# Kernel tuning notes

Hardware: AMD Instinct MI355X
Metric: run time of the kernel (lower is better)

## Reference

```python
import jax, jax.numpy as jnp
import numpy as np

B, S, D_MODEL, H = 2, 2048, 1024, 16
HD = D_MODEL // H  # 64
THETA = 10000.0


def setup_inputs() -> dict:
    key = jax.random.key(0)
    ks = jax.random.split(key, 5)
    std = (2.0 / (D_MODEL + D_MODEL)) ** 0.5
    x = jax.random.normal(ks[0], (B, S, D_MODEL), dtype=jnp.float32)
    Wq = jax.random.normal(ks[1], (D_MODEL, D_MODEL), dtype=jnp.float32) * std
    Wk = jax.random.normal(ks[2], (D_MODEL, D_MODEL), dtype=jnp.float32) * std
    Wv = jax.random.normal(ks[3], (D_MODEL, D_MODEL), dtype=jnp.float32) * std
    Wo = jax.random.normal(ks[4], (D_MODEL, D_MODEL), dtype=jnp.float32) * std
    # RoPE tables (buffers)
    pos = jnp.arange(S, dtype=jnp.float32)
    freq = THETA ** (-jnp.arange(0, HD, 2, dtype=jnp.float32) / HD)  # [HD/2]
    ang = jnp.outer(pos, freq)  # [S, HD/2]
    token_positions = jnp.arange(S, dtype=jnp.int32)
    return {
        "x": x,
        "token_positions": token_positions,
        "use_rope": 1,
        "Wq": Wq, "Wk": Wk, "Wv": Wv, "Wo": Wo,
        "cos": jnp.cos(ang), "sin": jnp.sin(ang),
    }


def _apply_rope(t, c, sn):
    # t: [b,h,s,d]; c,sn: [s,d/2] (broadcast over b,h)
    e = t[..., 0::2]
    o = t[..., 1::2]
    return jnp.stack([e * c - o * sn, o * c + e * sn], axis=-1).reshape(t.shape)


def reference(x, token_positions, use_rope, Wq, Wk, Wv, Wo, cos, sin):
    b, s, _ = x.shape

    def split_heads(t):  # [b,s,D] -> [b,h,s,hd]
        return t.reshape(b, s, H, HD).transpose(0, 2, 1, 3)

    q = split_heads(x @ Wq.T)
    k = split_heads(x @ Wk.T)
    v = split_heads(x @ Wv.T)

    if use_rope:
        c = cos[token_positions]   # [s, hd/2]
        sn = sin[token_positions]  # [s, hd/2]
        q = _apply_rope(q, c, sn)
        k = _apply_rope(k, c, sn)

    scale = 1.0 / jnp.sqrt(jnp.float32(HD))
    scores = jnp.einsum('bhqd,bhkd->bhqk', q, k) * scale  # [b,h,s,s]
    causal = jnp.tril(jnp.ones((s, s), dtype=bool))
    scores = jnp.where(causal, scores, -jnp.inf)
    attn = jax.nn.softmax(scores, axis=-1)
    y = jnp.einsum('bhqk,bhkd->bhqd', attn, v)
    y = y.transpose(0, 2, 1, 3).reshape(b, s, D_MODEL)
    return y @ Wo.T
```

## Files before the change

### kernel.cpp

```cpp
#include <hip/hip_runtime.h>
#include <math.h>

#define BB 2
#define SS 2048
#define DM 1024
#define NH 16
#define HD 64

typedef __attribute__((ext_vector_type(8))) __bf16 bf16x8;
typedef __attribute__((ext_vector_type(4))) __bf16 bf16x4;
typedef __attribute__((ext_vector_type(8))) unsigned short u16x8;
typedef __attribute__((ext_vector_type(4))) float f32x4;
typedef unsigned short u16;
typedef unsigned int u32;
typedef __attribute__((address_space(1))) unsigned int u32g;
typedef __attribute__((address_space(3))) unsigned int u32l;

#define CEXP 0.18033688011112042f

static __device__ __forceinline__ u16 f2bf(float f) {
    __bf16 h = (__bf16)f;
    return __builtin_bit_cast(unsigned short, h);
}

static __device__ __forceinline__ void gld16(const u16* g, u16* l) {
    __builtin_amdgcn_global_load_lds((const u32g*)g, (u32l*)l, 16, 0, 0);
}

__global__ __launch_bounds__(256)
void cast_all(const float* __restrict__ x,
              const float* __restrict__ wq, const float* __restrict__ wk,
              const float* __restrict__ wv, const float* __restrict__ wo,
              u16* __restrict__ xb, u16* __restrict__ wqb, u16* __restrict__ wkb,
              u16* __restrict__ wvb, u16* __restrict__ wob)
{
    const int N4X = (BB * SS * DM) / 4;
    const int N4W = (DM * DM) / 4;
    int i = blockIdx.x * 256 + threadIdx.x;
    const float* src; u16* dst; int off;
    if (i < N4X) { src = x; dst = xb; off = i; }
    else {
        int i2 = i - N4X;
        int w = i2 >> 18;
        off = i2 & (N4W - 1);
        switch (w) {
            case 0:  src = wq; dst = wqb; break;
            case 1:  src = wk; dst = wkb; break;
            case 2:  src = wv; dst = wvb; break;
            default: src = wo; dst = wob; break;
        }
    }
    float4 v = ((const float4*)src)[off];
    ushort4 o;
    o.x = f2bf(v.x); o.y = f2bf(v.y); o.z = f2bf(v.z); o.w = f2bf(v.w);
    ((ushort4*)dst)[off] = o;
}

__global__ __launch_bounds__(256)
void qkv_gemm(const u16* __restrict__ X,
              const u16* __restrict__ Wq, const u16* __restrict__ Wk,
              const u16* __restrict__ Wv,
              u16* __restrict__ Q, u16* __restrict__ K, u16* __restrict__ V)
{
    const u16* W; u16* dst;
    if (blockIdx.z == 0)      { W = Wq; dst = Q; }
    else if (blockIdx.z == 1) { W = Wk; dst = K; }
    else                      { W = Wv; dst = V; }

    __shared__ u16 As[128 * 32];
    __shared__ u16 Bs[128 * 32];
    const int t  = threadIdx.x;
    const int wv = t >> 6, L = t & 63, ln = L & 15, qd = L >> 4;
    const int i0 = blockIdx.y * 128, j0 = blockIdx.x * 128;
    const int wm = (wv >> 1) * 64, wn = (wv & 1) * 64;
    const int srow = L >> 2, scol = (L & 3) * 8;

    f32x4 acc[4][4];
    #pragma unroll
    for (int a = 0; a < 4; ++a)
        #pragma unroll
        for (int b = 0; b < 4; ++b)
            #pragma unroll
            for (int e = 0; e < 4; ++e) acc[a][b][e] = 0.f;

    for (int k0 = 0; k0 < DM; k0 += 32) {
        __syncthreads();
        gld16(X + (size_t)(i0 + wv * 32 +      srow) * DM + k0 + scol, &As[(wv * 32     ) * 32]);
        gld16(X + (size_t)(i0 + wv * 32 + 16 + srow) * DM + k0 + scol, &As[(wv * 32 + 16) * 32]);
        gld16(W + (size_t)(j0 + wv * 32 +      srow) * DM + k0 + scol, &Bs[(wv * 32     ) * 32]);
        gld16(W + (size_t)(j0 + wv * 32 + 16 + srow) * DM + k0 + scol, &Bs[(wv * 32 + 16) * 32]);
        __syncthreads();
        bf16x8 a[4], b[4];
        #pragma unroll
        for (int mi = 0; mi < 4; ++mi) a[mi] = *(const bf16x8*)&As[(wm + mi * 16 + ln) * 32 + qd * 8];
        #pragma unroll
        for (int ni = 0; ni < 4; ++ni) b[ni] = *(const bf16x8*)&Bs[(wn + ni * 16 + ln) * 32 + qd * 8];
        #pragma unroll
        for (int mi = 0; mi < 4; ++mi)
            #pragma unroll
            for (int ni = 0; ni < 4; ++ni)
                acc[mi][ni] = __builtin_amdgcn_mfma_f32_16x16x32_bf16(a[mi], b[ni], acc[mi][ni], 0, 0, 0);
    }

    #pragma unroll
    for (int mi = 0; mi < 4; ++mi)
        #pragma unroll
        for (int ni = 0; ni < 4; ++ni)
            #pragma unroll
            for (int r = 0; r < 4; ++r) {
                int gi = i0 + wm + mi * 16 + qd * 4 + r;
                int gj = j0 + wn + ni * 16 + ln;
                int b = gi >> 11, s = gi & 2047, h = gj >> 6, d = gj & 63;
                dst[(((size_t)(b * NH + h)) * SS + s) * HD + d] = f2bf(acc[mi][ni][r]);
            }
}

__global__ __launch_bounds__(256)
void out_gemm(const u16* __restrict__ X, const u16* __restrict__ W,
              float* __restrict__ dst)
{
    __shared__ u16 As[128 * 32];
    __shared__ u16 Bs[128 * 32];
    const int t  = threadIdx.x;
    const int wv = t >> 6, L = t & 63, ln = L & 15, qd = L >> 4;
    const int i0 = blockIdx.y * 128, j0 = blockIdx.x * 128;
    const int wm = (wv >> 1) * 64, wn = (wv & 1) * 64;
    const int srow = L >> 2, scol = (L & 3) * 8;

    f32x4 acc[4][4];
    #pragma unroll
    for (int a = 0; a < 4; ++a)
        #pragma unroll
        for (int b = 0; b < 4; ++b)
            #pragma unroll
            for (int e = 0; e < 4; ++e) acc[a][b][e] = 0.f;

    for (int k0 = 0; k0 < DM; k0 += 32) {
        __syncthreads();
        gld16(X + (size_t)(i0 + wv * 32 +      srow) * DM + k0 + scol, &As[(wv * 32     ) * 32]);
        gld16(X + (size_t)(i0 + wv * 32 + 16 + srow) * DM + k0 + scol, &As[(wv * 32 + 16) * 32]);
        gld16(W + (size_t)(j0 + wv * 32 +      srow) * DM + k0 + scol, &Bs[(wv * 32     ) * 32]);
        gld16(W + (size_t)(j0 + wv * 32 + 16 + srow) * DM + k0 + scol, &Bs[(wv * 32 + 16) * 32]);
        __syncthreads();
        bf16x8 a[4], b[4];
        #pragma unroll
        for (int mi = 0; mi < 4; ++mi) a[mi] = *(const bf16x8*)&As[(wm + mi * 16 + ln) * 32 + qd * 8];
        #pragma unroll
        for (int ni = 0; ni < 4; ++ni) b[ni] = *(const bf16x8*)&Bs[(wn + ni * 16 + ln) * 32 + qd * 8];
        #pragma unroll
        for (int mi = 0; mi < 4; ++mi)
            #pragma unroll
            for (int ni = 0; ni < 4; ++ni)
                acc[mi][ni] = __builtin_amdgcn_mfma_f32_16x16x32_bf16(a[mi], b[ni], acc[mi][ni], 0, 0, 0);
    }

    #pragma unroll
    for (int mi = 0; mi < 4; ++mi)
        #pragma unroll
        for (int ni = 0; ni < 4; ++ni)
            #pragma unroll
            for (int r = 0; r < 4; ++r) {
                int gi = i0 + wm + mi * 16 + qd * 4 + r;
                int gj = j0 + wn + ni * 16 + ln;
                dst[(size_t)gi * DM + gj] = acc[mi][ni][r];
            }
}

__global__ __launch_bounds__(256)
void rope_kernel(u16* __restrict__ Q, u16* __restrict__ Kt,
                 const int* __restrict__ tp, const float* __restrict__ cosp,
                 const float* __restrict__ sinp, const int* __restrict__ use_rope)
{
    if (use_rope[0] == 0) return;
    int idx = blockIdx.x * 256 + threadIdx.x;
    int p = idx & 31, s = (idx >> 5) & 2047, bh = idx >> 16;
    int pos = tp[s];
    float c  = cosp[pos * 32 + p];
    float sn = sinp[pos * 32 + p];
    size_t base = ((size_t)bh * SS + s) * HD + 2 * p;
    u32 qw = *(u32*)&Q[base];
    u32 kw = *(u32*)&Kt[base];
    float qe = __uint_as_float(qw << 16), qo = __uint_as_float(qw & 0xffff0000u);
    float ke = __uint_as_float(kw << 16), ko = __uint_as_float(kw & 0xffff0000u);
    u32 qn = (u32)f2bf(qe * c - qo * sn) | ((u32)f2bf(qo * c + qe * sn) << 16);
    u32 kn = (u32)f2bf(ke * c - ko * sn) | ((u32)f2bf(ko * c + ke * sn) << 16);
    *(u32*)&Q[base]  = qn;
    *(u32*)&Kt[base] = kn;
}

static __device__ __forceinline__ void group_step(
    const bf16x8 af[4][2], const bf16x8 qf[2], u16* psw,
    int diag, int rowg, int j0, int ln, int qd,
    float& m, float& l, f32x4* o, bf16x8& pf0, bf16x8& pf1)
{
    f32x4 s[4];
    #pragma unroll
    for (int mt = 0; mt < 4; ++mt) {
        #pragma unroll
        for (int e = 0; e < 4; ++e) s[mt][e] = 0.f;
        s[mt] = __builtin_amdgcn_mfma_f32_16x16x32_bf16(af[mt][0], qf[0], s[mt], 0, 0, 0);
        s[mt] = __builtin_amdgcn_mfma_f32_16x16x32_bf16(af[mt][1], qf[1], s[mt], 0, 0, 0);
    }
    if (diag) {
        #pragma unroll
        for (int mt = 0; mt < 4; ++mt)
            #pragma unroll
            for (int r = 0; r < 4; ++r)
                if (j0 + mt * 16 + qd * 4 + r > rowg) s[mt][r] = -3.0e38f;
    }
    float rm = s[0][0];
    #pragma unroll
    for (int mt = 0; mt < 4; ++mt)
        #pragma unroll
        for (int r = 0; r < 4; ++r) rm = fmaxf(rm, s[mt][r]);
    rm = fmaxf(rm, __shfl_xor(rm, 16));
    rm = fmaxf(rm, __shfl_xor(rm, 32));
    float nm = fmaxf(m, rm);
    float alpha = exp2f((m - nm) * CEXP);
    float nmc = nm * CEXP;
    float rs = 0.f;
    #pragma unroll
    for (int mt = 0; mt < 4; ++mt) {
        bf16x4 pk;
        #pragma unroll
        for (int r = 0; r < 4; ++r) {
            float pv = exp2f(fmaf(s[mt][r], CEXP, -nmc));
            rs += pv;
            pk[r] = (__bf16)pv;
        }
        *(bf16x4*)(psw + ln * 72 + mt * 16 + qd * 4) = pk;
    }
    rs += __shfl_xor(rs, 16);
    rs += __shfl_xor(rs, 32);
    l = l * alpha + rs;
    m = nm;
    #pragma unroll
    for (int r = 0; r < 4; ++r) {
        float ar = __shfl(alpha, qd * 4 + r);
        #pragma unroll
        for (int ni = 0; ni < 4; ++ni) o[ni][r] *= ar;
    }
    pf0 = *(const bf16x8*)(psw + ln * 72 + qd * 8);
    pf1 = *(const bf16x8*)(psw + ln * 72 + 32 + qd * 8);
}

__global__ __launch_bounds__(256, 2)
void attn_kernel(const u16* __restrict__ Q, const u16* __restrict__ K,
                 const u16* __restrict__ V, u16* __restrict__ Y)
{
    __shared__ u16 Ks[64 * 64];
    __shared__ u16 Vt[64 * 64];
    __shared__ u16 Ps[4][2][16 * 72];

    const int t  = threadIdx.x;
    const int wv = t >> 6, L = t & 63, ln = L & 15, qd = L >> 4;
    const int bh = blockIdx.x, p = blockIdx.y;
    const int qbA = p * 64, qbB = (31 - p) * 64;
    const u16* Qp = Q + (size_t)bh * SS * HD;
    const u16* Kp = K + (size_t)bh * SS * HD;
    const u16* Vp = V + (size_t)bh * SS * HD;

    bf16x8 qfA[2], qfB[2];
    {
        const u16* ra = Qp + (size_t)(qbA + wv * 16 + ln) * HD;
        qfA[0] = *(const bf16x8*)(ra + qd * 8);
        qfA[1] = *(const bf16x8*)(ra + 32 + qd * 8);
        const u16* rb = Qp + (size_t)(qbB + wv * 16 + ln) * HD;
        qfB[0] = *(const bf16x8*)(rb + qd * 8);
        qfB[1] = *(const bf16x8*)(rb + 32 + qd * 8);
    }

    f32x4 oA[4], oB[4];
    #pragma unroll
    for (int ni = 0; ni < 4; ++ni)
        #pragma unroll
        for (int e = 0; e < 4; ++e) { oA[ni][e] = 0.f; oB[ni][e] = 0.f; }
    float mA = -3.0e38f, lA = 0.f, mB = -3.0e38f, lB = 0.f;

    const int ntile = 32 - p;
    for (int tix = 0; tix < ntile; ++tix) {
        const int j0 = tix * 64;
        __syncthreads();
        #pragma unroll
        for (int cc = 0; cc < 2; ++cc) {
            int c = t + cc * 256;
            int kr = c >> 3, c8 = c & 7;
            u16x8 val = *(const u16x8*)(Kp + (size_t)(j0 + kr) * HD + c8 * 8);
            *(u16x8*)&Ks[kr * 64 + ((c8 ^ (kr & 7)) * 8)] = val;
        }
        {
            int kp = t & 31, dg = t >> 5;
            const u16* v0 = Vp + (size_t)(j0 + 2 * kp) * HD + dg * 8;
            u16x8 va = *(const u16x8*)v0;
            u16x8 vb = *(const u16x8*)(v0 + HD);
            #pragma unroll
            for (int u = 0; u < 8; ++u) {
                int d = dg * 8 + u;
                u32 w = (u32)va[u] | ((u32)vb[u] << 16);
                *(u32*)&Vt[d * 64 + ((kp >> 2) ^ (d & 7)) * 8 + 2 * (kp & 3)] = w;
            }
        }
        __syncthreads();

        bf16x8 af[4][2];
        #pragma unroll
        for (int mt = 0; mt < 4; ++mt)
            #pragma unroll
            for (int kc = 0; kc < 2; ++kc)
                af[mt][kc] = *(const bf16x8*)&Ks[(mt * 16 + ln) * 64 + (((kc * 4 + qd) ^ (ln & 7)) * 8)];

        const bool hasA = (tix <= p);
        bf16x8 pA0, pA1, pB0, pB1;
        if (hasA)
            group_step(af, qfA, &Ps[wv][0][0], tix == p, qbA + wv * 16 + ln, j0, ln, qd,
                       mA, lA, oA, pA0, pA1);
        group_step(af, qfB, &Ps[wv][1][0], tix == ntile - 1, qbB + wv * 16 + ln, j0, ln, qd,
                   mB, lB, oB, pB0, pB1);

        #pragma unroll
        for (int kc = 0; kc < 2; ++kc)
            #pragma unroll
            for (int ni = 0; ni < 4; ++ni) {
                bf16x8 vf = *(const bf16x8*)&Vt[(ni * 16 + ln) * 64 + (((kc * 4 + qd) ^ (ln & 7)) * 8)];
                if (hasA)
                    oA[ni] = __builtin_amdgcn_mfma_f32_16x16x32_bf16(kc ? pA1 : pA0, vf, oA[ni], 0, 0, 0);
                oB[ni] = __builtin_amdgcn_mfma_f32_16x16x32_bf16(kc ? pB1 : pB0, vf, oB[ni], 0, 0, 0);
            }
    }

    const int b = bh >> 4, h = bh & 15;
    #pragma unroll
    for (int r = 0; r < 4; ++r) {
        float invA = 1.f / __shfl(lA, qd * 4 + r);
        float invB = 1.f / __shfl(lB, qd * 4 + r);
        int sA = qbA + wv * 16 + qd * 4 + r;
        int sB = qbB + wv * 16 + qd * 4 + r;
        #pragma unroll
        for (int ni = 0; ni < 4; ++ni) {
            int d = ni * 16 + ln;
            Y[((size_t)(b * SS + sA)) * DM + h * HD + d] = f2bf(oA[ni][r] * invA);
            Y[((size_t)(b * SS + sB)) * DM + h * HD + d] = f2bf(oB[ni][r] * invB);
        }
    }
}

extern "C" void kernel_launch(void* const* d_in, const int* in_sizes, int n_in,
                              void* d_out, int out_size, void* d_ws, size_t ws_size,
                              hipStream_t stream)
{
    const float* x        = (const float*)d_in[0];
    const int*   tp       = (const int*)d_in[1];
    const int*   use_rope = (const int*)d_in[2];
    const float* Wq       = (const float*)d_in[3];
    const float* Wk       = (const float*)d_in[4];
    const float* Wv       = (const float*)d_in[5];
    const float* Wo       = (const float*)d_in[6];
    const float* cosp     = (const float*)d_in[7];
    const float* sinp     = (const float*)d_in[8];
    float* out = (float*)d_out;

    char* ws = (char*)d_ws;
    const size_t MB = 1 << 20;
    u16* xb  = (u16*)(ws);
    u16* Wqb = (u16*)(ws + 8 * MB);
    u16* Wkb = (u16*)(ws + 10 * MB);
    u16* Wvb = (u16*)(ws + 12 * MB);
    u16* Wob = (u16*)(ws + 14 * MB);
    u16* Qb  = (u16*)(ws + 16 * MB);
    u16* Kb  = (u16*)(ws + 24 * MB);
    u16* Vb  = (u16*)(ws + 32 * MB);
    u16* Yb  = (u16*)(ws + 40 * MB);

    cast_all<<<8192, 256, 0, stream>>>(x, Wq, Wk, Wv, Wo, xb, Wqb, Wkb, Wvb, Wob);
    qkv_gemm<<<dim3(DM / 128, BB * SS / 128, 3), 256, 0, stream>>>(xb, Wqb, Wkb, Wvb, Qb, Kb, Vb);
    rope_kernel<<<(BB * NH * SS * 32) / 256, 256, 0, stream>>>(Qb, Kb, tp, cosp, sinp, use_rope);
    attn_kernel<<<dim3(BB * NH, 16), 256, 0, stream>>>(Qb, Kb, Vb, Yb);
    out_gemm<<<dim3(DM / 128, BB * SS / 128), 256, 0, stream>>>(Yb, Wob, out);
}
```

Measured before the change: 211.0 us.

## Fuse RoPE into QKV GEMM, retile GEMMs, pipeline K/V loads in attention

The QKV projection now computes Q, K and V together in one kernel that shares the X tile across all three weights, and applies RoPE in its epilogue using lane-pair shuffles. This removes the separate rope kernel and its extra read and write of Q and K. Both GEMMs move to 128x64 tiles with a minimum of two blocks per CU, which gives the out_gemm more blocks. In attention, K fragments are now loaded straight from global memory into registers, and V is double-buffered in LDS so the next tile's loads overlap the current compute, at the cost of more register pressure.

```diff
diff --git a/kernel.cpp b/kernel.cpp
--- a/kernel.cpp
+++ b/kernel.cpp
@@ -56,136 +56,137 @@
     ((ushort4*)dst)[off] = o;
 }
 
-__global__ __launch_bounds__(256)
-void qkv_gemm(const u16* __restrict__ X,
-              const u16* __restrict__ Wq, const u16* __restrict__ Wk,
-              const u16* __restrict__ Wv,
-              u16* __restrict__ Q, u16* __restrict__ K, u16* __restrict__ V)
-{
-    const u16* W; u16* dst;
-    if (blockIdx.z == 0)      { W = Wq; dst = Q; }
-    else if (blockIdx.z == 1) { W = Wk; dst = K; }
-    else                      { W = Wv; dst = V; }
-
+__global__ __launch_bounds__(256, 2)
+void qkv_fused(const u16* __restrict__ X,
+               const u16* __restrict__ Wq, const u16* __restrict__ Wk,
+               const u16* __restrict__ Wv,
+               const int* __restrict__ tp, const float* __restrict__ cosp,
+               const float* __restrict__ sinp, const int* __restrict__ use_rope,
+               u16* __restrict__ Q, u16* __restrict__ K, u16* __restrict__ V)
+{
     __shared__ u16 As[128 * 32];
-    __shared__ u16 Bs[128 * 32];
+    __shared__ u16 Bs[3][64 * 32];
     const int t  = threadIdx.x;
     const int wv = t >> 6, L = t & 63, ln = L & 15, qd = L >> 4;
-    const int i0 = blockIdx.y * 128, j0 = blockIdx.x * 128;
-    const int wm = (wv >> 1) * 64, wn = (wv & 1) * 64;
+    const int i0 = blockIdx.y * 128, j0 = blockIdx.x * 64;
+    const int wm = (wv >> 1) * 64, wn = (wv & 1) * 32;
     const int srow = L >> 2, scol = (L & 3) * 8;
 
-    f32x4 acc[4][4];
-    #pragma unroll
-    for (int a = 0; a < 4; ++a)
-        #pragma unroll
-        for (int b = 0; b < 4; ++b)
-            #pragma unroll
-            for (int e = 0; e < 4; ++e) acc[a][b][e] = 0.f;
+    f32x4 acc[3][4][2];
+    #pragma unroll
+    for (int w = 0; w < 3; ++w)
+        #pragma unroll
+        for (int mi = 0; mi < 4; ++mi)
+            #pragma unroll
+            for (int ni = 0; ni < 2; ++ni)
+                #pragma unroll
+                for (int e = 0; e < 4; ++e) acc[w][mi][ni][e] = 0.f;
+
+    for (int k0 = 0; k0 < DM; k0 += 32) {
+        __syncthreads();
+        gld16(X  + (size_t)(i0 + wv * 32 +      srow) * DM + k0 + scol, &As[(wv * 32     ) * 32]);
+        gld16(X  + (size_t)(i0 + wv * 32 + 16 + srow) * DM + k0 + scol, &As[(wv * 32 + 16) * 32]);
+        gld16(Wq + (size_t)(j0 + wv * 16 +      srow) * DM + k0 + scol, &Bs[0][(wv * 16) * 32]);
+        gld16(Wk + (size_t)(j0 + wv * 16 +      srow) * DM + k0 + scol, &Bs[1][(wv * 16) * 32]);
+        gld16(Wv + (size_t)(j0 + wv * 16 +      srow) * DM + k0 + scol, &Bs[2][(wv * 16) * 32]);
+        __syncthreads();
+        bf16x8 a[4];
+        #pragma unroll
+        for (int mi = 0; mi < 4; ++mi) a[mi] = *(const bf16x8*)&As[(wm + mi * 16 + ln) * 32 + qd * 8];
+        bf16x8 b[3][2];
+        #pragma unroll
+        for (int w = 0; w < 3; ++w)
+            #pragma unroll
+            for (int ni = 0; ni < 2; ++ni)
+                b[w][ni] = *(const bf16x8*)&Bs[w][(wn + ni * 16 + ln) * 32 + qd * 8];
+        #pragma unroll
+        for (int w = 0; w < 3; ++w)
+            #pragma unroll
+            for (int mi = 0; mi < 4; ++mi)
+                #pragma unroll
+                for (int ni = 0; ni < 2; ++ni)
+                    acc[w][mi][ni] = __builtin_amdgcn_mfma_f32_16x16x32_bf16(a[mi], b[w][ni], acc[w][mi][ni], 0, 0, 0);
+    }
+
+    const int rope_on = use_rope[0];
+    #pragma unroll
+    for (int mi = 0; mi < 4; ++mi)
+        #pragma unroll
+        for (int r = 0; r < 4; ++r) {
+            int gi = i0 + wm + mi * 16 + qd * 4 + r;
+            int b_ = gi >> 11, s = gi & 2047;
+            int pos = tp[s];
+            #pragma unroll
+            for (int ni = 0; ni < 2; ++ni) {
+                int gj = j0 + wn + ni * 16 + ln;
+                int h = gj >> 6, d = gj & 63;
+                size_t oidx = (((size_t)(b_ * NH + h)) * SS + s) * HD + d;
+                float qv = acc[0][mi][ni][r];
+                float kv = acc[1][mi][ni][r];
+                float qp = __shfl_xor(qv, 1);
+                float kp = __shfl_xor(kv, 1);
+                if (rope_on) {
+                    int p = d >> 1;
+                    float c  = cosp[pos * 32 + p];
+                    float sn = sinp[pos * 32 + p];
+                    if (d & 1) { qv = qv * c + qp * sn; kv = kv * c + kp * sn; }
+                    else       { qv = qv * c - qp * sn; kv = kv * c - kp * sn; }
+                }
+                Q[oidx] = f2bf(qv);
+                K[oidx] = f2bf(kv);
+                V[oidx] = f2bf(acc[2][mi][ni][r]);
+            }
+        }
+}
+
+__global__ __launch_bounds__(256, 2)
+void out_gemm(const u16* __restrict__ X, const u16* __restrict__ W,
+              float* __restrict__ dst)
+{
+    __shared__ u16 As[128 * 32];
+    __shared__ u16 Bs[64 * 32];
+    const int t  = threadIdx.x;
+    const int wv = t >> 6, L = t & 63, ln = L & 15, qd = L >> 4;
+    const int i0 = blockIdx.y * 128, j0 = blockIdx.x * 64;
+    const int wm = (wv >> 1) * 64, wn = (wv & 1) * 32;
+    const int srow = L >> 2, scol = (L & 3) * 8;
+
+    f32x4 acc[4][2];
+    #pragma unroll
+    for (int mi = 0; mi < 4; ++mi)
+        #pragma unroll
+        for (int ni = 0; ni < 2; ++ni)
+            #pragma unroll
+            for (int e = 0; e < 4; ++e) acc[mi][ni][e] = 0.f;
 
     for (int k0 = 0; k0 < DM; k0 += 32) {
         __syncthreads();
         gld16(X + (size_t)(i0 + wv * 32 +      srow) * DM + k0 + scol, &As[(wv * 32     ) * 32]);
         gld16(X + (size_t)(i0 + wv * 32 + 16 + srow) * DM + k0 + scol, &As[(wv * 32 + 16) * 32]);
-        gld16(W + (size_t)(j0 + wv * 32 +      srow) * DM + k0 + scol, &Bs[(wv * 32     ) * 32]);
-        gld16(W + (size_t)(j0 + wv * 32 + 16 + srow) * DM + k0 + scol, &Bs[(wv * 32 + 16) * 32]);
+        gld16(W + (size_t)(j0 + wv * 16 +      srow) * DM + k0 + scol, &Bs[(wv * 16) * 32]);
         __syncthreads();
-        bf16x8 a[4], b[4];
+        bf16x8 a[4], b[2];
         #pragma unroll
         for (int mi = 0; mi < 4; ++mi) a[mi] = *(const bf16x8*)&As[(wm + mi * 16 + ln) * 32 + qd * 8];
         #pragma unroll
-        for (int ni = 0; ni < 4; ++ni) b[ni] = *(const bf16x8*)&Bs[(wn + ni * 16 + ln) * 32 + qd * 8];
+        for (int ni = 0; ni < 2; ++ni) b[ni] = *(const bf16x8*)&Bs[(wn + ni * 16 + ln) * 32 + qd * 8];
         #pragma unroll
         for (int mi = 0; mi < 4; ++mi)
             #pragma unroll
-            for (int ni = 0; ni < 4; ++ni)
+            for (int ni = 0; ni < 2; ++ni)
                 acc[mi][ni] = __builtin_amdgcn_mfma_f32_16x16x32_bf16(a[mi], b[ni], acc[mi][ni], 0, 0, 0);
     }
 
     #pragma unroll
     for (int mi = 0; mi < 4; ++mi)
         #pragma unroll
-        for (int ni = 0; ni < 4; ++ni)
-            #pragma unroll
-            for (int r = 0; r < 4; ++r) {
-                int gi = i0 + wm + mi * 16 + qd * 4 + r;
-                int gj = j0 + wn + ni * 16 + ln;
-                int b = gi >> 11, s = gi & 2047, h = gj >> 6, d = gj & 63;
-                dst[(((size_t)(b * NH + h)) * SS + s) * HD + d] = f2bf(acc[mi][ni][r]);
-            }
-}
-
-__global__ __launch_bounds__(256)
-void out_gemm(const u16* __restrict__ X, const u16* __restrict__ W,
-              float* __restrict__ dst)
-{
-    __shared__ u16 As[128 * 32];
-    __shared__ u16 Bs[128 * 32];
-    const int t  = threadIdx.x;
-    const int wv = t >> 6, L = t & 63, ln = L & 15, qd = L >> 4;
-    const int i0 = blockIdx.y * 128, j0 = blockIdx.x * 128;
-    const int wm = (wv >> 1) * 64, wn = (wv & 1) * 64;
-    const int srow = L >> 2, scol = (L & 3) * 8;
-
-    f32x4 acc[4][4];
-    #pragma unroll
-    for (int a = 0; a < 4; ++a)
-        #pragma unroll
-        for (int b = 0; b < 4; ++b)
-            #pragma unroll
-            for (int e = 0; e < 4; ++e) acc[a][b][e] = 0.f;
-
-    for (int k0 = 0; k0 < DM; k0 += 32) {
-        __syncthreads();
-        gld16(X + (size_t)(i0 + wv * 32 +      srow) * DM + k0 + scol, &As[(wv * 32     ) * 32]);
-        gld16(X + (size_t)(i0 + wv * 32 + 16 + srow) * DM + k0 + scol, &As[(wv * 32 + 16) * 32]);
-        gld16(W + (size_t)(j0 + wv * 32 +      srow) * DM + k0 + scol, &Bs[(wv * 32     ) * 32]);
-        gld16(W + (size_t)(j0 + wv * 32 + 16 + srow) * DM + k0 + scol, &Bs[(wv * 32 + 16) * 32]);
-        __syncthreads();
-        bf16x8 a[4], b[4];
-        #pragma unroll
-        for (int mi = 0; mi < 4; ++mi) a[mi] = *(const bf16x8*)&As[(wm + mi * 16 + ln) * 32 + qd * 8];
-        #pragma unroll
-        for (int ni = 0; ni < 4; ++ni) b[ni] = *(const bf16x8*)&Bs[(wn + ni * 16 + ln) * 32 + qd * 8];
-        #pragma unroll
-        for (int mi = 0; mi < 4; ++mi)
-            #pragma unroll
-            for (int ni = 0; ni < 4; ++ni)
-                acc[mi][ni] = __builtin_amdgcn_mfma_f32_16x16x32_bf16(a[mi], b[ni], acc[mi][ni], 0, 0, 0);
-    }
-
-    #pragma unroll
-    for (int mi = 0; mi < 4; ++mi)
-        #pragma unroll
-        for (int ni = 0; ni < 4; ++ni)
+        for (int ni = 0; ni < 2; ++ni)
             #pragma unroll
             for (int r = 0; r < 4; ++r) {
                 int gi = i0 + wm + mi * 16 + qd * 4 + r;
                 int gj = j0 + wn + ni * 16 + ln;
                 dst[(size_t)gi * DM + gj] = acc[mi][ni][r];
             }
-}
-
-__global__ __launch_bounds__(256)
-void rope_kernel(u16* __restrict__ Q, u16* __restrict__ Kt,
-                 const int* __restrict__ tp, const float* __restrict__ cosp,
-                 const float* __restrict__ sinp, const int* __restrict__ use_rope)
-{
-    if (use_rope[0] == 0) return;
-    int idx = blockIdx.x * 256 + threadIdx.x;
-    int p = idx & 31, s = (idx >> 5) & 2047, bh = idx >> 16;
-    int pos = tp[s];
-    float c  = cosp[pos * 32 + p];
-    float sn = sinp[pos * 32 + p];
-    size_t base = ((size_t)bh * SS + s) * HD + 2 * p;
-    u32 qw = *(u32*)&Q[base];
-    u32 kw = *(u32*)&Kt[base];
-    float qe = __uint_as_float(qw << 16), qo = __uint_as_float(qw & 0xffff0000u);
-    float ke = __uint_as_float(kw << 16), ko = __uint_as_float(kw & 0xffff0000u);
-    u32 qn = (u32)f2bf(qe * c - qo * sn) | ((u32)f2bf(qo * c + qe * sn) << 16);
-    u32 kn = (u32)f2bf(ke * c - ko * sn) | ((u32)f2bf(ko * c + ke * sn) << 16);
-    *(u32*)&Q[base]  = qn;
-    *(u32*)&Kt[base] = kn;
 }
 
 static __device__ __forceinline__ void group_step(
@@ -248,8 +249,7 @@
 void attn_kernel(const u16* __restrict__ Q, const u16* __restrict__ K,
                  const u16* __restrict__ V, u16* __restrict__ Y)
 {
-    __shared__ u16 Ks[64 * 64];
-    __shared__ u16 Vt[64 * 64];
+    __shared__ u16 Vt[2][64 * 64];
     __shared__ u16 Ps[4][2][16 * 72];
 
     const int t  = threadIdx.x;
@@ -259,6 +259,7 @@
     const u16* Qp = Q + (size_t)bh * SS * HD;
     const u16* Kp = K + (size_t)bh * SS * HD;
     const u16* Vp = V + (size_t)bh * SS * HD;
+    const int vkp = t & 31, vdg = t >> 5;
 
     bf16x8 qfA[2], qfB[2];
     {
@@ -278,36 +279,43 @@
     float mA = -3.0e38f, lA = 0.f, mB = -3.0e38f, lB = 0.f;
 
     const int ntile = 32 - p;
+
+    {
+        const u16* v0 = Vp + (size_t)(2 * vkp) * HD + vdg * 8;
+        u16x8 va = *(const u16x8*)v0;
+        u16x8 vb = *(const u16x8*)(v0 + HD);
+        #pragma unroll
+        for (int u = 0; u < 8; ++u) {
+            int d = vdg * 8 + u;
+            u32 w = (u32)va[u] | ((u32)vb[u] << 16);
+            *(u32*)&Vt[0][d * 64 + ((vkp >> 2) ^ (d & 7)) * 8 + 2 * (vkp & 3)] = w;
+        }
+    }
+    bf16x8 af[4][2];
+    #pragma unroll
+    for (int mt = 0; mt < 4; ++mt)
+        #pragma unroll
+        for (int kc = 0; kc < 2; ++kc)
+            af[mt][kc] = *(const bf16x8*)(Kp + (size_t)(mt * 16 + ln) * HD + kc * 32 + qd * 8);
+    __syncthreads();
+
     for (int tix = 0; tix < ntile; ++tix) {
         const int j0 = tix * 64;
-        __syncthreads();
-        #pragma unroll
-        for (int cc = 0; cc < 2; ++cc) {
-            int c = t + cc * 256;
-            int kr = c >> 3, c8 = c & 7;
-            u16x8 val = *(const u16x8*)(Kp + (size_t)(j0 + kr) * HD + c8 * 8);
-            *(u16x8*)&Ks[kr * 64 + ((c8 ^ (kr & 7)) * 8)] = val;
-        }
-        {
-            int kp = t & 31, dg = t >> 5;
-            const u16* v0 = Vp + (size_t)(j0 + 2 * kp) * HD + dg * 8;
-            u16x8 va = *(const u16x8*)v0;
-            u16x8 vb = *(const u16x8*)(v0 + HD);
-            #pragma unroll
-            for (int u = 0; u < 8; ++u) {
-                int d = dg * 8 + u;
-                u32 w = (u32)va[u] | ((u32)vb[u] << 16);
-                *(u32*)&Vt[d * 64 + ((kp >> 2) ^ (d & 7)) * 8 + 2 * (kp & 3)] = w;
-            }
-        }
-        __syncthreads();
-
-        bf16x8 af[4][2];
-        #pragma unroll
-        for (int mt = 0; mt < 4; ++mt)
-            #pragma unroll
-            for (int kc = 0; kc < 2; ++kc)
-                af[mt][kc] = *(const bf16x8*)&Ks[(mt * 16 + ln) * 64 + (((kc * 4 + qd) ^ (ln & 7)) * 8)];
+        const int buf = tix & 1;
+        const bool more = (tix + 1 < ntile);
+
+        u16x8 nva, nvb;
+        bf16x8 afn[4][2];
+        if (more) {
+            const u16* v0 = Vp + (size_t)(j0 + 64 + 2 * vkp) * HD + vdg * 8;
+            nva = *(const u16x8*)v0;
+            nvb = *(const u16x8*)(v0 + HD);
+            #pragma unroll
+            for (int mt = 0; mt < 4; ++mt)
+                #pragma unroll
+                for (int kc = 0; kc < 2; ++kc)
+                    afn[mt][kc] = *(const bf16x8*)(Kp + (size_t)(j0 + 64 + mt * 16 + ln) * HD + kc * 32 + qd * 8);
+        }
 
         const bool hasA = (tix <= p);
         bf16x8 pA0, pA1, pB0, pB1;
@@ -321,11 +329,26 @@
         for (int kc = 0; kc < 2; ++kc)
             #pragma unroll
             for (int ni = 0; ni < 4; ++ni) {
-                bf16x8 vf = *(const bf16x8*)&Vt[(ni * 16 + ln) * 64 + (((kc * 4 + qd) ^ (ln & 7)) * 8)];
+                bf16x8 vf = *(const bf16x8*)&Vt[buf][(ni * 16 + ln) * 64 + (((kc * 4 + qd) ^ (ln & 7)) * 8)];
                 if (hasA)
                     oA[ni] = __builtin_amdgcn_mfma_f32_16x16x32_bf16(kc ? pA1 : pA0, vf, oA[ni], 0, 0, 0);
                 oB[ni] = __builtin_amdgcn_mfma_f32_16x16x32_bf16(kc ? pB1 : pB0, vf, oB[ni], 0, 0, 0);
             }
+
+        if (more) {
+            #pragma unroll
+            for (int u = 0; u < 8; ++u) {
+                int d = vdg * 8 + u;
+                u32 w = (u32)nva[u] | ((u32)nvb[u] << 16);
+                *(u32*)&Vt[buf ^ 1][d * 64 + ((vkp >> 2) ^ (d & 7)) * 8 + 2 * (vkp & 3)] = w;
+            }
+            #pragma unroll
+            for (int mt = 0; mt < 4; ++mt)
+                #pragma unroll
+                for (int kc = 0; kc < 2; ++kc)
+                    af[mt][kc] = afn[mt][kc];
+        }
+        __syncthreads();
     }
 
     const int b = bh >> 4, h = bh & 15;
@@ -372,8 +395,8 @@
     u16* Yb  = (u16*)(ws + 40 * MB);
 
     cast_all<<<8192, 256, 0, stream>>>(x, Wq, Wk, Wv, Wo, xb, Wqb, Wkb, Wvb, Wob);
-    qkv_gemm<<<dim3(DM / 128, BB * SS / 128, 3), 256, 0, stream>>>(xb, Wqb, Wkb, Wvb, Qb, Kb, Vb);
-    rope_kernel<<<(BB * NH * SS * 32) / 256, 256, 0, stream>>>(Qb, Kb, tp, cosp, sinp, use_rope);
+    qkv_fused<<<dim3(DM / 64, BB * SS / 128), 256, 0, stream>>>(
+        xb, Wqb, Wkb, Wvb, tp, cosp, sinp, use_rope, Qb, Kb, Vb);
     attn_kernel<<<dim3(BB * NH, 16), 256, 0, stream>>>(Qb, Kb, Vb, Yb);
-    out_gemm<<<dim3(DM / 128, BB * SS / 128), 256, 0, stream>>>(Yb, Wob, out);
-}
+    out_gemm<<<dim3(DM / 64, BB * SS / 128), 256, 0, stream>>>(Yb, Wob, out);
+}
```

New measurement: 229.8 us. 8.9% more time.
